# Kernel optimization log

Hardware: AMD Instinct MI355X
Metric: run time of the kernel (lower is better)

The kernel has to match this reference:

```python
import jax, jax.numpy as jnp
import numpy as np

GROUP_SIZE = 128


def _dequant_groupwise(values, scales, group_size):
    # values: [rows, cols] int codes; scales: [rows, cols//group_size]
    rows, cols = values.shape
    groups = cols // group_size  # dims chosen to divide evenly (no padding branch)
    v = values.astype(jnp.float32).reshape(rows, groups, group_size)
    return (v * scales[:, :, None]).reshape(rows, cols)


def setup_inputs() -> dict:
    key = jax.random.key(0)
    ks = jax.random.split(key, 8)
    tokens, d_in, d_out, rank = 8192, 4096, 4096, 256
    return {
        "x": jax.random.normal(ks[0], (tokens, d_in), dtype=jnp.float32),
        "q_values": jax.random.randint(ks[1], (d_out, d_in), 0, 16, dtype=jnp.int32),
        "q_scales": jax.random.uniform(ks[2], (d_out, d_in // GROUP_SIZE), dtype=jnp.float32),
        "l_values": jax.random.randint(ks[3], (d_out, rank), 0, 16, dtype=jnp.int32),
        "l_scales": jax.random.uniform(ks[4], (d_out, rank // GROUP_SIZE), dtype=jnp.float32),
        "r_values": jax.random.randint(ks[5], (rank, d_in), 0, 16, dtype=jnp.int32),
        "r_scales": jax.random.uniform(ks[6], (rank, d_in // GROUP_SIZE), dtype=jnp.float32),
        "bias": jax.random.normal(ks[7], (d_out,), dtype=jnp.float32),
    }


def reference(x, q_values, q_scales, l_values, l_scales, r_values, r_scales, bias):
    # Dequantize groupwise int-quantized weights, then y = x @ Q^T + (x @ R^T) @ L^T + b
    q = _dequant_groupwise(q_values, q_scales, GROUP_SIZE)  # [out, in]
    l = _dequant_groupwise(l_values, l_scales, GROUP_SIZE)  # [out, rank]
    r = _dequant_groupwise(r_values, r_scales, GROUP_SIZE)  # [rank, in]
    xr = jnp.einsum('ti,ri->tr', x, r)          # [tokens, rank]
    base = jnp.einsum('ti,oi->to', x, q)        # [tokens, out]
    low_rank = jnp.einsum('tr,or->to', xr, l)   # [tokens, out]
    return base + low_rank + bias
```

## Files before the change

kernel.cpp:

```cpp
#include <hip/hip_runtime.h>
#include <cstdint>
#include <cstddef>

typedef float f32x4 __attribute__((ext_vector_type(4)));
typedef __bf16 bf16x8 __attribute__((ext_vector_type(8)));

__device__ __forceinline__ unsigned short f2bf(float f) {
    unsigned int u = __float_as_uint(f);
    u += 0x7fffu + ((u >> 16) & 1u);
    return (unsigned short)(u >> 16);
}

__device__ __forceinline__ void async_copy16(const void* g, void* l) {
    __builtin_amdgcn_global_load_lds(
        (__attribute__((address_space(1))) void*)(g),
        (__attribute__((address_space(3))) void*)(l), 16, 0, 0);
}

__global__ void prep_kernel(const float* __restrict__ x,
                            unsigned short* __restrict__ xb,
                            const int* __restrict__ lv,
                            const float* __restrict__ ls,
                            unsigned short* __restrict__ Ld,
                            const int* __restrict__ rv,
                            const float* __restrict__ rs,
                            unsigned short* __restrict__ Rt) {
    const int bid = blockIdx.x;
    const int tid = threadIdx.x;
    if (bid < 16384) {
        const int i = bid * 256 + tid;
        const float4* xv = (const float4*)x;
        float4 a = xv[2 * (size_t)i];
        float4 b = xv[2 * (size_t)i + 1];
        union { unsigned short u[8]; uint4 v; } r;
        r.u[0] = f2bf(a.x); r.u[1] = f2bf(a.y); r.u[2] = f2bf(a.z); r.u[3] = f2bf(a.w);
        r.u[4] = f2bf(b.x); r.u[5] = f2bf(b.y); r.u[6] = f2bf(b.z); r.u[7] = f2bf(b.w);
        ((uint4*)xb)[i] = r.v;
    } else if (bid < 16896) {
        const int i = (bid - 16384) * 256 + tid;
        const int e = i * 8;
        const int row = e >> 8;
        const int col = e & 255;
        const float sc = ls[row * 2 + (col >> 7)];
        int4 a = ((const int4*)lv)[2 * (size_t)i];
        int4 b = ((const int4*)lv)[2 * (size_t)i + 1];
        union { unsigned short u[8]; uint4 v; } r;
        r.u[0] = f2bf(a.x * sc); r.u[1] = f2bf(a.y * sc);
        r.u[2] = f2bf(a.z * sc); r.u[3] = f2bf(a.w * sc);
        r.u[4] = f2bf(b.x * sc); r.u[5] = f2bf(b.y * sc);
        r.u[6] = f2bf(b.z * sc); r.u[7] = f2bf(b.w * sc);
        ((uint4*)Ld)[i] = r.v;
    } else {
        const int g = (bid - 16896) * 256 + tid;
        const int i  = g & 4095;
        const int r0 = (g >> 12) << 3;
        const int grp = i >> 7;
        union { unsigned short u[8]; uint4 v; } w;
        #pragma unroll
        for (int k = 0; k < 8; ++k) {
            const int r = r0 + k;
            const float sc = rs[r * 32 + grp];
            w.u[k] = f2bf((float)rv[(size_t)r * 4096 + i] * sc);
        }
        *(uint4*)&Rt[(size_t)i * 256 + r0] = w.v;
    }
}


#define SM_OFF(slot_, mat_, half_) ((((slot_) * 2 + (mat_)) * 2 + (half_)) * 8192)

#define MFMA_QUAD(MG, NG, AA, BB)                                           \
    _Pragma("unroll")                                                       \
    for (int m_ = 0; m_ < 4; ++m_)                                          \
        _Pragma("unroll")                                                   \
        for (int n_ = 0; n_ < 2; ++n_)                                      \
            _Pragma("unroll")                                               \
            for (int k_ = 0; k_ < 2; ++k_)                                  \
                acc[(MG)*4 + m_][(NG)*2 + n_] =                             \
                    __builtin_amdgcn_mfma_f32_16x16x32_bf16(                \
                        AA[m_][k_], BB[n_][k_],                             \
                        acc[(MG)*4 + m_][(NG)*2 + n_], 0, 0, 0)

#define PH_SYNC()                                                            \
    __builtin_amdgcn_s_barrier();                                            \
    asm volatile("s_waitcnt lgkmcnt(0)" ::: "memory")

__device__ __forceinline__ void run_pipeline(
    const __bf16* __restrict__ A, const __bf16* __restrict__ B,
    const int lda, const int nt,
    const int mBase, const int nBase,
    const int wave, const int lane, const int wr, const int wc,
    __bf16* smp, f32x4 (&acc)[8][4])
{
    const int lrow  = lane >> 3;
    const int lcol  = (((lane & 7) ^ lrow) & 7) * 8;
    const int soff0 = (wave * 8 + lrow) * lda + lcol;
    const size_t dsoff = (size_t)64 * lda;

    const __bf16* gA0 = A + (size_t)mBase * lda + soff0;
    const __bf16* gA1 = gA0 + (size_t)128 * lda;
    const __bf16* gB0 = B + (size_t)nBase * lda + soff0;
    const __bf16* gB1 = gB0 + (size_t)128 * lda;

    const int aoff0 = (lane & 15) * 64 + ((((lane >> 4))     ^ (lane & 7)) * 8);
    const int aoff1 = (lane & 15) * 64 + (((4 + (lane >> 4)) ^ (lane & 7)) * 8);

    const __bf16* Ah0 = smp + SM_OFF(0, 0, wr);
    const __bf16* Ah1 = smp + SM_OFF(1, 0, wr);
    const __bf16* Bh0 = smp + SM_OFF(0, 1, wc >> 1) + (wc & 1) * 4096;
    const __bf16* Bh1 = smp + SM_OFF(1, 1, wc >> 1) + (wc & 1) * 4096;

#define STAGE(gp_, tile_, slot_, mat_, half_) do {                           \
        const __bf16* g_ = (gp_) + (size_t)(tile_) * 64;                     \
        __bf16* d_ = smp + SM_OFF(slot_, mat_, half_);                       \
        async_copy16(g_,         d_ + wave * 512);                           \
        async_copy16(g_ + dsoff, d_ + (wave + 8) * 512);                     \
    } while (0)

    STAGE(gB0, 0, 0, 1, 0);
    STAGE(gB1, 0, 0, 1, 1);
    STAGE(gA0, 0, 0, 0, 0);
    STAGE(gA1, 0, 0, 0, 1);
    STAGE(gB0, 1, 1, 1, 0);
    STAGE(gB1, 1, 1, 1, 1);
    STAGE(gA0, 1, 1, 0, 0);
    asm volatile("s_waitcnt vmcnt(6)" ::: "memory");
    __builtin_amdgcn_s_barrier();

    bf16x8 aR[4][2], bLo[2][2], bHi[2][2];

    const int niter = nt >> 1;
    #pragma unroll 1
    for (int i = 0; i < niter; ++i) {
        const int t1 = 2 * i + 1;
        int p2 = 2 * i + 2; if (p2 >= nt) p2 = nt - 2;
        int p3 = 2 * i + 3; if (p3 >= nt) p3 = nt - 1;

        #pragma unroll
        for (int m = 0; m < 4; ++m) {
            aR[m][0] = *(const bf16x8*)(Ah0 + m * 1024 + aoff0);
            aR[m][1] = *(const bf16x8*)(Ah0 + m * 1024 + aoff1);
        }
        #pragma unroll
        for (int n = 0; n < 2; ++n) {
            bLo[n][0] = *(const bf16x8*)(Bh0 + n * 1024 + aoff0);
            bLo[n][1] = *(const bf16x8*)(Bh0 + n * 1024 + aoff1);
        }
        STAGE(gA1, t1, 1, 0, 1);
        PH_SYNC();
        __builtin_amdgcn_s_setprio(1);
        MFMA_QUAD(0, 0, aR, bLo);
        __builtin_amdgcn_s_setprio(0);

        #pragma unroll
        for (int n = 0; n < 2; ++n) {
            bHi[n][0] = *(const bf16x8*)(Bh0 + (2 + n) * 1024 + aoff0);
            bHi[n][1] = *(const bf16x8*)(Bh0 + (2 + n) * 1024 + aoff1);
        }
        STAGE(gB0, p2, 0, 1, 0);
        PH_SYNC();
        __builtin_amdgcn_s_setprio(1);
        MFMA_QUAD(0, 1, aR, bHi);
        __builtin_amdgcn_s_setprio(0);

        #pragma unroll
        for (int m = 0; m < 4; ++m) {
            aR[m][0] = *(const bf16x8*)(Ah0 + (4 + m) * 1024 + aoff0);
            aR[m][1] = *(const bf16x8*)(Ah0 + (4 + m) * 1024 + aoff1);
        }
        STAGE(gB1, p2, 0, 1, 1);
        PH_SYNC();
        __builtin_amdgcn_s_setprio(1);
        MFMA_QUAD(1, 1, aR, bHi);
        __builtin_amdgcn_s_setprio(0);

        STAGE(gA0, p2, 0, 0, 0);
        asm volatile("s_waitcnt vmcnt(6)" ::: "memory");
        __builtin_amdgcn_s_barrier();
        __builtin_amdgcn_s_setprio(1);
        MFMA_QUAD(1, 0, aR, bLo);
        __builtin_amdgcn_s_setprio(0);

        #pragma unroll
        for (int m = 0; m < 4; ++m) {
            aR[m][0] = *(const bf16x8*)(Ah1 + m * 1024 + aoff0);
            aR[m][1] = *(const bf16x8*)(Ah1 + m * 1024 + aoff1);
        }
        #pragma unroll
        for (int n = 0; n < 2; ++n) {
            bLo[n][0] = *(const bf16x8*)(Bh1 + n * 1024 + aoff0);
            bLo[n][1] = *(const bf16x8*)(Bh1 + n * 1024 + aoff1);
        }
        STAGE(gA1, p2, 0, 0, 1);
        PH_SYNC();
        __builtin_amdgcn_s_setprio(1);
        MFMA_QUAD(0, 0, aR, bLo);
        __builtin_amdgcn_s_setprio(0);

        #pragma unroll
        for (int n = 0; n < 2; ++n) {
            bHi[n][0] = *(const bf16x8*)(Bh1 + (2 + n) * 1024 + aoff0);
            bHi[n][1] = *(const bf16x8*)(Bh1 + (2 + n) * 1024 + aoff1);
        }
        STAGE(gB0, p3, 1, 1, 0);
        PH_SYNC();
        __builtin_amdgcn_s_setprio(1);
        MFMA_QUAD(0, 1, aR, bHi);
        __builtin_amdgcn_s_setprio(0);

        #pragma unroll
        for (int m = 0; m < 4; ++m) {
            aR[m][0] = *(const bf16x8*)(Ah1 + (4 + m) * 1024 + aoff0);
            aR[m][1] = *(const bf16x8*)(Ah1 + (4 + m) * 1024 + aoff1);
        }
        STAGE(gB1, p3, 1, 1, 1);
        PH_SYNC();
        __builtin_amdgcn_s_setprio(1);
        MFMA_QUAD(1, 1, aR, bHi);
        __builtin_amdgcn_s_setprio(0);

        STAGE(gA0, p3, 1, 0, 0);
        asm volatile("s_waitcnt vmcnt(6)" ::: "memory");
        __builtin_amdgcn_s_barrier();
        __builtin_amdgcn_s_setprio(1);
        MFMA_QUAD(1, 0, aR, bLo);
        __builtin_amdgcn_s_setprio(0);
    }

    asm volatile("s_waitcnt vmcnt(0)" ::: "memory");
    __builtin_amdgcn_s_barrier();
#undef STAGE
}

__global__ void __launch_bounds__(512, 2)
lr_w_kernel(const __bf16* __restrict__ Ld,
            const __bf16* __restrict__ Rt,
            const int*   __restrict__ qv,
            const float* __restrict__ qs,
            unsigned short* __restrict__ Wp)
{
    __shared__ __bf16 sm[2][2][2][8192];
    const int tid  = threadIdx.x;
    const int lane = tid & 63;
    const int wave = tid >> 6;
    const int wr = wave >> 2;
    const int wc = wave & 3;

    const int bid = blockIdx.x;
    const int cpx = gridDim.x >> 3;
    const int s   = (bid & 7) * cpx + (bid >> 3);
    const int mBase = (s >> 4) * 256;
    const int nBase = (s & 15) * 256;

    f32x4 acc[8][4] = {};
    __bf16* smp = &sm[0][0][0][0];
    run_pipeline(Ld, Rt, 256, 4, mBase, nBase, wave, lane, wr, wc, smp, acc);

    float* lsm = (float*)smp;
    const int cn = lane & 15;
    const int rg = (lane >> 4) * 4;

    #pragma unroll 1
    for (int h = 0; h < 2; ++h) {
        #pragma unroll
        for (int mf4 = 0; mf4 < 4; ++mf4) {
            const int mf = h * 4 + mf4;
            #pragma unroll
            for (int nf = 0; nf < 4; ++nf) {
                #pragma unroll
                for (int r = 0; r < 4; ++r) {
                    const int lrowi = wr * 64 + mf4 * 16 + rg + r;
                    const int col = (wc * 64 + nf * 16 + cn) ^ (((lrowi >> 2) & 1) << 4);
                    lsm[lrowi * 256 + col] = acc[mf][nf][r];
                }
            }
        }
        __syncthreads();
        #pragma unroll 2
        for (int it = 0; it < 8; ++it) {
            const int linear = it * 512 + tid;
            const int lrowi  = linear >> 5;
            const int coff   = (linear & 31) * 8;
            const int grow = mBase + ((lrowi >> 6) * 128) + h * 64 + (lrowi & 63);
            const int gcol = nBase + coff;
            const int cswz = (coff * 4) ^ (((lrowi >> 2) & 1) << 6);
            const float* lp = (const float*)((const char*)lsm + (size_t)lrowi * 1024 + cswz);
            f32x4 lo = *(const f32x4*)lp;
            f32x4 hi = *(const f32x4*)(lp + 4);
            const float sc = qs[grow * 32 + (gcol >> 7)];
            const int4 qa = *(const int4*)&qv[(size_t)grow * 4096 + gcol];
            const int4 qb = *(const int4*)&qv[(size_t)grow * 4096 + gcol + 4];
            union { unsigned short u[8]; uint4 x; } w;
            w.u[0] = f2bf(qa.x * sc + lo[0]);
            w.u[1] = f2bf(qa.y * sc + lo[1]);
            w.u[2] = f2bf(qa.z * sc + lo[2]);
            w.u[3] = f2bf(qa.w * sc + lo[3]);
            w.u[4] = f2bf(qb.x * sc + hi[0]);
            w.u[5] = f2bf(qb.y * sc + hi[1]);
            w.u[6] = f2bf(qb.z * sc + hi[2]);
            w.u[7] = f2bf(qb.w * sc + hi[3]);
            *(uint4*)&Wp[(size_t)grow * 4096 + gcol] = w.x;
        }
        __syncthreads();
    }
}

__global__ void __launch_bounds__(512, 2)
gemm256_kernel(const __bf16* __restrict__ A, const __bf16* __restrict__ B,
               int lda, int nt,
               const float* __restrict__ bias, float* __restrict__ out,
               int ldo, int gxlog2) {
    __shared__ __bf16 sm[2][2][2][8192];

    const int tid  = threadIdx.x;
    const int lane = tid & 63;
    const int wave = tid >> 6;
    const int wr = wave >> 2;
    const int wc = wave & 3;

    const int bid = blockIdx.x;
    const int cpx = gridDim.x >> 3;
    const int s   = (bid & 7) * cpx + (bid >> 3);
    const int bx  = s & ((1 << gxlog2) - 1);
    const int by  = s >> gxlog2;
    const int mBase = by * 256;
    const int nBase = bx * 256;

    f32x4 acc[8][4] = {};
    __bf16* smp = &sm[0][0][0][0];
    run_pipeline(A, B, lda, nt, mBase, nBase, wave, lane, wr, wc, smp, acc);

    const int cn = lane & 15;
    const int rg = (lane >> 4) * 4;
    const int row0 = mBase + wr * 128 + rg;
    const int col0 = nBase + wc * 64 + cn;
    #pragma unroll
    for (int nf = 0; nf < 4; ++nf) {
        const int o = col0 + nf * 16;
        const float bv = bias[o];
        #pragma unroll
        for (int mf = 0; mf < 8; ++mf) {
            const int t0 = row0 + mf * 16;
            #pragma unroll
            for (int r = 0; r < 4; ++r)
                out[(size_t)(t0 + r) * ldo + o] = acc[mf][nf][r] + bv;
        }
    }
}

extern "C" void kernel_launch(void* const* d_in, const int* in_sizes, int n_in,
                              void* d_out, int out_size, void* d_ws, size_t ws_size,
                              hipStream_t stream) {
    const float* x    = (const float*)d_in[0];
    const int*   qv   = (const int*)d_in[1];
    const float* qs   = (const float*)d_in[2];
    const int*   lv   = (const int*)d_in[3];
    const float* ls   = (const float*)d_in[4];
    const int*   rv   = (const int*)d_in[5];
    const float* rs   = (const float*)d_in[6];
    const float* bias = (const float*)d_in[7];
    float* out = (float*)d_out;

    const int T = 8192, DI = 4096, DO = 4096;

    char* ws = (char*)d_ws;
    unsigned short* xb = (unsigned short*)(ws);
    unsigned short* Wp = (unsigned short*)(ws + 67108864);
    unsigned short* Ld = (unsigned short*)(ws + 100663296);
    unsigned short* Rt = (unsigned short*)(ws + 102760448);

    {
        prep_kernel<<<17408, 256, 0, stream>>>(
            x, xb, lv, ls, Ld, rv, rs, Rt);
    }
    {
        lr_w_kernel<<<256, 512, 0, stream>>>(
            (const __bf16*)Ld, (const __bf16*)Rt, qv, qs, Wp);
    }
    {
        int nblocks = (DO / 256) * (T / 256);
        gemm256_kernel<<<nblocks, 512, 0, stream>>>(
            (const __bf16*)xb, (const __bf16*)Wp, DI, DI / 64,
            bias, out, DO, 4 );
    }
}
```

Before: 541.2 us.

## Prefetch LDS fragments during MFMA phases and remap blocks to XCD-local tiles

Restructures the GEMM main loop so that LDS-to-register reads for the next phase are issued after the current MFMA quad instead of before it. Extra register sets (aLo/aHi, bLo0/bLo1) double-buffer the fragments so LDS latency overlaps matrix math. The per-phase barrier now sits at the end of each phase and the vmcnt waits move. Separately, the block-to-tile mapping is replaced with a fixed scheme that gives each XCD an 8x8 tile region for better L2 locality. That mapping assumes a 16x32 grid, and the extra fragment registers raise register pressure under 512 threads with 2 blocks per CU.

```diff
diff --git a/kernel.cpp b/kernel.cpp
--- a/kernel.cpp
+++ b/kernel.cpp
@@ -81,9 +81,25 @@
                         AA[m_][k_], BB[n_][k_],                             \
                         acc[(MG)*4 + m_][(NG)*2 + n_], 0, 0, 0)
 
-#define PH_SYNC()                                                            \
-    __builtin_amdgcn_s_barrier();                                            \
-    asm volatile("s_waitcnt lgkmcnt(0)" ::: "memory")
+#define RD_A(dst_, src_, base_)                                             \
+    _Pragma("unroll")                                                       \
+    for (int m_ = 0; m_ < 4; ++m_) {                                        \
+        dst_[m_][0] = *(const bf16x8*)((src_) + ((base_) + m_) * 1024 + aoff0); \
+        dst_[m_][1] = *(const bf16x8*)((src_) + ((base_) + m_) * 1024 + aoff1); \
+    }
+
+#define RD_B(dst_, src_, base_)                                             \
+    _Pragma("unroll")                                                       \
+    for (int n_ = 0; n_ < 2; ++n_) {                                        \
+        dst_[n_][0] = *(const bf16x8*)((src_) + ((base_) + n_) * 1024 + aoff0); \
+        dst_[n_][1] = *(const bf16x8*)((src_) + ((base_) + n_) * 1024 + aoff1); \
+    }
+
+#define PH_TOP()                                                            \
+    asm volatile("s_waitcnt lgkmcnt(0)" ::: "memory");                      \
+    __builtin_amdgcn_sched_barrier(0)
+
+#define PH_END() __builtin_amdgcn_s_barrier()
 
 __device__ __forceinline__ void run_pipeline(
     const __bf16* __restrict__ A, const __bf16* __restrict__ B,
@@ -127,7 +143,10 @@
     asm volatile("s_waitcnt vmcnt(6)" ::: "memory");
     __builtin_amdgcn_s_barrier();
 
-    bf16x8 aR[4][2], bLo[2][2], bHi[2][2];
+    bf16x8 aLo[4][2], aHi[4][2], bLo0[2][2], bLo1[2][2], bHi[2][2];
+
+    RD_A(aLo, Ah0, 0);
+    RD_B(bLo0, Bh0, 0);
 
     const int niter = nt >> 1;
     #pragma unroll 1
@@ -136,99 +155,76 @@
         int p2 = 2 * i + 2; if (p2 >= nt) p2 = nt - 2;
         int p3 = 2 * i + 3; if (p3 >= nt) p3 = nt - 1;
 
-        #pragma unroll
-        for (int m = 0; m < 4; ++m) {
-            aR[m][0] = *(const bf16x8*)(Ah0 + m * 1024 + aoff0);
-            aR[m][1] = *(const bf16x8*)(Ah0 + m * 1024 + aoff1);
-        }
-        #pragma unroll
-        for (int n = 0; n < 2; ++n) {
-            bLo[n][0] = *(const bf16x8*)(Bh0 + n * 1024 + aoff0);
-            bLo[n][1] = *(const bf16x8*)(Bh0 + n * 1024 + aoff1);
-        }
+        PH_TOP();
+        __builtin_amdgcn_s_setprio(1);
+        MFMA_QUAD(0, 0, aLo, bLo0);
+        __builtin_amdgcn_s_setprio(0);
+        RD_B(bHi, Bh0, 2);
         STAGE(gA1, t1, 1, 0, 1);
-        PH_SYNC();
-        __builtin_amdgcn_s_setprio(1);
-        MFMA_QUAD(0, 0, aR, bLo);
-        __builtin_amdgcn_s_setprio(0);
-
-        #pragma unroll
-        for (int n = 0; n < 2; ++n) {
-            bHi[n][0] = *(const bf16x8*)(Bh0 + (2 + n) * 1024 + aoff0);
-            bHi[n][1] = *(const bf16x8*)(Bh0 + (2 + n) * 1024 + aoff1);
-        }
+        PH_END();
+
+        PH_TOP();
+        __builtin_amdgcn_s_setprio(1);
+        MFMA_QUAD(0, 1, aLo, bHi);
+        __builtin_amdgcn_s_setprio(0);
+        RD_A(aHi, Ah0, 4);
         STAGE(gB0, p2, 0, 1, 0);
-        PH_SYNC();
-        __builtin_amdgcn_s_setprio(1);
-        MFMA_QUAD(0, 1, aR, bHi);
-        __builtin_amdgcn_s_setprio(0);
-
-        #pragma unroll
-        for (int m = 0; m < 4; ++m) {
-            aR[m][0] = *(const bf16x8*)(Ah0 + (4 + m) * 1024 + aoff0);
-            aR[m][1] = *(const bf16x8*)(Ah0 + (4 + m) * 1024 + aoff1);
-        }
+        PH_END();
+
+        PH_TOP();
+        __builtin_amdgcn_s_setprio(1);
+        MFMA_QUAD(1, 1, aHi, bHi);
+        __builtin_amdgcn_s_setprio(0);
+        asm volatile("s_waitcnt vmcnt(2)" ::: "memory");
+        RD_A(aLo, Ah1, 0);
+        RD_B(bLo1, Bh1, 0);
         STAGE(gB1, p2, 0, 1, 1);
-        PH_SYNC();
-        __builtin_amdgcn_s_setprio(1);
-        MFMA_QUAD(1, 1, aR, bHi);
-        __builtin_amdgcn_s_setprio(0);
-
+        PH_END();
+
+        PH_TOP();
+        __builtin_amdgcn_s_setprio(1);
+        MFMA_QUAD(1, 0, aHi, bLo0);
+        __builtin_amdgcn_s_setprio(0);
+        RD_B(bHi, Bh1, 2);
         STAGE(gA0, p2, 0, 0, 0);
-        asm volatile("s_waitcnt vmcnt(6)" ::: "memory");
-        __builtin_amdgcn_s_barrier();
-        __builtin_amdgcn_s_setprio(1);
-        MFMA_QUAD(1, 0, aR, bLo);
-        __builtin_amdgcn_s_setprio(0);
-
-        #pragma unroll
-        for (int m = 0; m < 4; ++m) {
-            aR[m][0] = *(const bf16x8*)(Ah1 + m * 1024 + aoff0);
-            aR[m][1] = *(const bf16x8*)(Ah1 + m * 1024 + aoff1);
-        }
-        #pragma unroll
-        for (int n = 0; n < 2; ++n) {
-            bLo[n][0] = *(const bf16x8*)(Bh1 + n * 1024 + aoff0);
-            bLo[n][1] = *(const bf16x8*)(Bh1 + n * 1024 + aoff1);
-        }
+        PH_END();
+
+        PH_TOP();
+        __builtin_amdgcn_s_setprio(1);
+        MFMA_QUAD(0, 0, aLo, bLo1);
+        __builtin_amdgcn_s_setprio(0);
+        RD_A(aHi, Ah1, 4);
         STAGE(gA1, p2, 0, 0, 1);
-        PH_SYNC();
-        __builtin_amdgcn_s_setprio(1);
-        MFMA_QUAD(0, 0, aR, bLo);
-        __builtin_amdgcn_s_setprio(0);
-
-        #pragma unroll
-        for (int n = 0; n < 2; ++n) {
-            bHi[n][0] = *(const bf16x8*)(Bh1 + (2 + n) * 1024 + aoff0);
-            bHi[n][1] = *(const bf16x8*)(Bh1 + (2 + n) * 1024 + aoff1);
-        }
+        PH_END();
+
+        PH_TOP();
+        __builtin_amdgcn_s_setprio(1);
+        MFMA_QUAD(0, 1, aLo, bHi);
+        __builtin_amdgcn_s_setprio(0);
         STAGE(gB0, p3, 1, 1, 0);
-        PH_SYNC();
-        __builtin_amdgcn_s_setprio(1);
-        MFMA_QUAD(0, 1, aR, bHi);
-        __builtin_amdgcn_s_setprio(0);
-
-        #pragma unroll
-        for (int m = 0; m < 4; ++m) {
-            aR[m][0] = *(const bf16x8*)(Ah1 + (4 + m) * 1024 + aoff0);
-            aR[m][1] = *(const bf16x8*)(Ah1 + (4 + m) * 1024 + aoff1);
-        }
+        PH_END();
+
+        PH_TOP();
+        __builtin_amdgcn_s_setprio(1);
+        MFMA_QUAD(1, 1, aHi, bHi);
+        __builtin_amdgcn_s_setprio(0);
+        asm volatile("s_waitcnt vmcnt(2)" ::: "memory");
+        RD_A(aLo, Ah0, 0);
+        RD_B(bLo0, Bh0, 0);
         STAGE(gB1, p3, 1, 1, 1);
-        PH_SYNC();
-        __builtin_amdgcn_s_setprio(1);
-        MFMA_QUAD(1, 1, aR, bHi);
-        __builtin_amdgcn_s_setprio(0);
-
+        PH_END();
+
+        PH_TOP();
+        __builtin_amdgcn_s_setprio(1);
+        MFMA_QUAD(1, 0, aHi, bLo1);
+        __builtin_amdgcn_s_setprio(0);
         STAGE(gA0, p3, 1, 0, 0);
-        asm volatile("s_waitcnt vmcnt(6)" ::: "memory");
-        __builtin_amdgcn_s_barrier();
-        __builtin_amdgcn_s_setprio(1);
-        MFMA_QUAD(1, 0, aR, bLo);
-        __builtin_amdgcn_s_setprio(0);
+        PH_END();
     }
 
     asm volatile("s_waitcnt vmcnt(0)" ::: "memory");
     __builtin_amdgcn_s_barrier();
+    asm volatile("s_waitcnt lgkmcnt(0)" ::: "memory");
 #undef STAGE
 }
 
@@ -309,7 +305,7 @@
 gemm256_kernel(const __bf16* __restrict__ A, const __bf16* __restrict__ B,
                int lda, int nt,
                const float* __restrict__ bias, float* __restrict__ out,
-               int ldo, int gxlog2) {
+               int ldo) {
     __shared__ __bf16 sm[2][2][2][8192];
 
     const int tid  = threadIdx.x;
@@ -319,10 +315,10 @@
     const int wc = wave & 3;
 
     const int bid = blockIdx.x;
-    const int cpx = gridDim.x >> 3;
-    const int s   = (bid & 7) * cpx + (bid >> 3);
-    const int bx  = s & ((1 << gxlog2) - 1);
-    const int by  = s >> gxlog2;
+    const int xcd = bid & 7;
+    const int u   = bid >> 3;
+    const int bx  = (xcd & 1) * 8 + (u & 7);
+    const int by  = (xcd >> 1) * 8 + (u >> 3);
     const int mBase = by * 256;
     const int nBase = bx * 256;
 
@@ -381,6 +377,6 @@
         int nblocks = (DO / 256) * (T / 256);
         gemm256_kernel<<<nblocks, 512, 0, stream>>>(
             (const __bf16*)xb, (const __bf16*)Wp, DI, DI / 64,
-            bias, out, DO, 4 );
-    }
-}
+            bias, out, DO);
+    }
+}
```

Result: slower. 968.9 us (+79.0%).
